# Kernel tuning notes

Hardware: AMD Instinct MI355X
Metric: run time of the kernel (lower is better)

## Reference

```python
import jax, jax.numpy as jnp
import numpy as np

EMBED_DIM = 400
NUM_HEADS = 4
HEAD_SIZE = EMBED_DIM // NUM_HEADS  # 100


def setup_inputs() -> dict:
    key = jax.random.key(0)
    ks = jax.random.split(key, 6)
    B, T = 8, 2048
    x = jax.random.normal(ks[0], (B, T, EMBED_DIM), dtype=jnp.float32)
    # per-head projection weights, stacked over heads: [H, C, D]
    scale = 1.0 / np.sqrt(EMBED_DIM)
    Wq = jax.random.normal(ks[1], (NUM_HEADS, EMBED_DIM, HEAD_SIZE), dtype=jnp.float32) * scale
    Wk = jax.random.normal(ks[2], (NUM_HEADS, EMBED_DIM, HEAD_SIZE), dtype=jnp.float32) * scale
    Wv = jax.random.normal(ks[3], (NUM_HEADS, EMBED_DIM, HEAD_SIZE), dtype=jnp.float32) * scale
    Wo = jax.random.normal(ks[4], (EMBED_DIM, EMBED_DIM), dtype=jnp.float32) * scale
    bo = jax.random.normal(ks[5], (EMBED_DIM,), dtype=jnp.float32) * scale
    return {"x": x, "Wq": Wq, "Wk": Wk, "Wv": Wv, "Wo": Wo, "bo": bo}


def reference(x, Wq, Wk, Wv, Wo, bo):
    B, T, C = x.shape
    inv_sqrt_d = 1.0 / jnp.sqrt(jnp.asarray(HEAD_SIZE, x.dtype))
    # project: [B,T,C] x [H,C,D] -> [B,H,T,D]
    q = jnp.einsum('btc,hcd->bhtd', x, Wq)
    k = jnp.einsum('btc,hcd->bhtd', x, Wk)
    v = jnp.einsum('btc,hcd->bhtd', x, Wv)
    scores = jnp.einsum('bhtd,bhsd->bhts', q, k) * inv_sqrt_d  # [B,H,T,T]
    causal = jnp.tril(jnp.ones((T, T), dtype=bool))
    scores = jnp.where(causal, scores, -jnp.inf)
    attn = jax.nn.softmax(scores, axis=-1)
    out = jnp.einsum('bhts,bhsd->bhtd', attn, v)  # [B,H,T,D]
    # concat heads (head order matches torch concat on last dim)
    out = out.transpose(0, 2, 1, 3).reshape(B, T, C)
    # output projection; dropout is identity in eval mode
    return out @ Wo.T + bo
```

## Files before the change

### kernel.cpp

```cpp
#include <hip/hip_runtime.h>
#include <hip/hip_bf16.h>

#define B_ 8
#define T_ 2048
#define C_ 400
#define H_ 4
#define D_ 100
#define DP 128
#define KP 416
#define KPB 832
#define QSCALE 0.14426950408889634f
#define MSTATIC 16.0f

typedef __hip_bfloat16 bf16;
typedef unsigned int uint32;
typedef __attribute__((ext_vector_type(8))) short short8;
typedef __attribute__((ext_vector_type(4))) float f32x4;

__device__ __forceinline__ float bf2f(bf16 v){ return __bfloat162float(v); }
__device__ __forceinline__ bf16 f2bf(float f){ return __float2bfloat16(f); }
__device__ __forceinline__ unsigned short bfbits(float f){
  bf16 h = f2bf(f);
  return __builtin_bit_cast(unsigned short, h);
}
__device__ __forceinline__ uint32 pk2(float a, float b){
  return (uint32)bfbits(a) | ((uint32)bfbits(b) << 16);
}
__device__ __forceinline__ void gl_lds16(const char* gsrc, char* ldst){
  __builtin_amdgcn_global_load_lds(
      (const __attribute__((address_space(1))) unsigned int*)gsrc,
      (__attribute__((address_space(3))) unsigned int*)ldst, 16, 0, 0);
}

__global__ __launch_bounds__(256) void conv_x_kernel(const float* __restrict__ x,
    bf16* __restrict__ xb){
  int i = blockIdx.x*256 + threadIdx.x;
  if (i >= 16384*52) return;
  int c8 = i % 52, t = i / 52;
  uint32 u[4];
  if (c8 < 50){
    const float* src = x + (size_t)t*C_ + c8*8;
    #pragma unroll
    for (int k=0;k<4;++k) u[k] = pk2(src[2*k], src[2*k+1]);
  } else {
    u[0]=u[1]=u[2]=u[3]=0;
  }
  *reinterpret_cast<uint4*>((char*)xb + (size_t)t*KPB + c8*16) = make_uint4(u[0],u[1],u[2],u[3]);
}

__global__ __launch_bounds__(256) void prep_wqkv_kernel(const float* __restrict__ Wq,
    const float* __restrict__ Wk, const float* __restrict__ Wv, bf16* __restrict__ WT){
  int i = blockIdx.x*256 + threadIdx.x;
  if (i >= 12*128*KP) return;
  int c = i % KP, n = (i/KP) & 127, group = i/(KP*128);
  int p = group >> 2, h = group & 3;
  float v = 0.f;
  if (n < D_ && c < C_){
    const float* W = (p==0)?Wq:(p==1)?Wk:Wv;
    v = W[((size_t)h*C_ + c)*D_ + n];
  }
  WT[i] = f2bf(v);
}

__global__ __launch_bounds__(256) void prep_wo_kernel(const float* __restrict__ Wo,
    bf16* __restrict__ WoB){
  int i = blockIdx.x*256 + threadIdx.x;
  if (i >= 512*KP) return;
  int c = i % KP, n = i / KP;
  float v = (n < C_ && c < C_) ? Wo[(size_t)n*C_ + c] : 0.f;
  WoB[i] = f2bf(v);
}

__global__ __launch_bounds__(256) void qkv_gemm_kernel(const bf16* __restrict__ xb,
    const bf16* __restrict__ WT, bf16* __restrict__ Qp, bf16* __restrict__ Kp,
    bf16* __restrict__ VT){
  __shared__ __align__(16) char xs[2][8192];
  __shared__ __align__(16) char wsh[2][8192];
  int bid = blockIdx.x;
  int xcd = bid & 7, idx = bid >> 3;
  int mb = xcd*16 + idx/12;
  int group = idx % 12;
  int p = group >> 2, h = group & 3;
  int t0 = mb * 128;
  int tid = threadIdx.x;
  int w = tid >> 6, l = tid & 63, g = l >> 4, qi = l & 15;
  const char* xg = (const char*)xb + (size_t)t0*KPB;
  const char* wg = (const char*)WT + (size_t)group*128*KPB;
  int srow = tid >> 2, sseg = tid & 3;

  #define GSTAGE(J, BUF) {                                                     \
    int kc2 = (J)*64;                                                          \
    _Pragma("unroll")                                                          \
    for (int r2=0;r2<2;++r2)                                                   \
      gl_lds16(xg + (size_t)(srow + r2*64)*KPB + kc2 + sseg*16,                \
               &xs[BUF][tid*16 + r2*4096]);                                    \
    _Pragma("unroll")                                                          \
    for (int r2=0;r2<2;++r2)                                                   \
      gl_lds16(wg + (size_t)(srow + r2*64)*KPB + kc2 + sseg*16,                \
               &wsh[BUF][tid*16 + r2*4096]); }

  f32x4 acc[2][8];
  #pragma unroll
  for (int mt=0;mt<2;++mt)
    #pragma unroll
    for (int nt=0;nt<8;++nt) acc[mt][nt] = (f32x4){0.f,0.f,0.f,0.f};

  GSTAGE(0, 0)
  __syncthreads();
  for (int j = 0; j < 13; ++j){
    int cur = j & 1;
    if (j < 12) GSTAGE(j+1, cur^1)
    short8 af[2];
    #pragma unroll
    for (int mt=0;mt<2;++mt)
      af[mt] = *reinterpret_cast<const short8*>(&xs[cur][(w*32 + mt*16 + qi)*64 + g*16]);
    short8 bfr[8];
    #pragma unroll
    for (int nt=0;nt<8;++nt)
      bfr[nt] = *reinterpret_cast<const short8*>(&wsh[cur][(nt*16 + qi)*64 + g*16]);
    if (p < 2){
      #pragma unroll
      for (int mt=0;mt<2;++mt)
        #pragma unroll
        for (int nt=0;nt<8;++nt)
          acc[mt][nt] = __builtin_amdgcn_mfma_f32_16x16x32_bf16(af[mt], bfr[nt], acc[mt][nt], 0,0,0);
    } else {
      #pragma unroll
      for (int mt=0;mt<2;++mt)
        #pragma unroll
        for (int nt=0;nt<8;++nt)
          acc[mt][nt] = __builtin_amdgcn_mfma_f32_16x16x32_bf16(bfr[nt], af[mt], acc[mt][nt], 0,0,0);
    }
    __syncthreads();
  }

  int b = t0 >> 11, tloc0 = t0 & 2047;
  size_t bh = (size_t)b*H_ + h;
  if (p < 2){
    float qs = (p==0) ? QSCALE : 1.0f;
    bf16* dst = (p==0 ? Qp : Kp) + (bh*T_ + tloc0)*DP;
    #pragma unroll
    for (int mt=0;mt<2;++mt)
      #pragma unroll
      for (int r=0;r<4;++r){
        int tr = w*32 + mt*16 + 4*g + r;
        #pragma unroll
        for (int nt=0;nt<8;++nt)
          dst[(size_t)tr*DP + nt*16 + qi] = f2bf(qs * acc[mt][nt][r]);
      }
  } else {
    bf16* dstv = VT + bh*DP*T_ + tloc0;
    #pragma unroll
    for (int nt=0;nt<8;++nt)
      #pragma unroll
      for (int r=0;r<4;++r){
        int d = nt*16 + 4*g + r;
        #pragma unroll
        for (int mt=0;mt<2;++mt)
          dstv[(size_t)d*T_ + w*32 + mt*16 + qi] = f2bf(acc[mt][nt][r]);
      }
  }
  #undef GSTAGE
}

__global__ __launch_bounds__(256) void out_gemm_kernel(const bf16* __restrict__ AOb,
    const bf16* __restrict__ WoB, const float* __restrict__ bo, float* __restrict__ out){
  __shared__ __align__(16) char xs[2][8192];
  __shared__ __align__(16) char wsh[2][8192];
  int bid = blockIdx.x;
  int xcd = bid & 7, idx = bid >> 3;
  int mb = xcd*16 + idx/4;
  int nb = idx & 3;
  int t0 = mb * 128, n0 = nb * 128;
  int tid = threadIdx.x;
  int w = tid >> 6, l = tid & 63, g = l >> 4, qi = l & 15;
  const char* xg = (const char*)AOb + (size_t)t0*KPB;
  const char* wg = (const char*)WoB + (size_t)n0*KPB;
  int srow = tid >> 2, sseg = tid & 3;

  #define GSTAGE(J, BUF) {                                                     \
    int kc2 = (J)*64;                                                          \
    _Pragma("unroll")                                                          \
    for (int r2=0;r2<2;++r2)                                                   \
      gl_lds16(xg + (size_t)(srow + r2*64)*KPB + kc2 + sseg*16,                \
               &xs[BUF][tid*16 + r2*4096]);                                    \
    _Pragma("unroll")                                                          \
    for (int r2=0;r2<2;++r2)                                                   \
      gl_lds16(wg + (size_t)(srow + r2*64)*KPB + kc2 + sseg*16,                \
               &wsh[BUF][tid*16 + r2*4096]); }

  f32x4 acc[2][8];
  #pragma unroll
  for (int mt=0;mt<2;++mt)
    #pragma unroll
    for (int nt=0;nt<8;++nt) acc[mt][nt] = (f32x4){0.f,0.f,0.f,0.f};

  GSTAGE(0, 0)
  __syncthreads();
  for (int j = 0; j < 13; ++j){
    int cur = j & 1;
    if (j < 12) GSTAGE(j+1, cur^1)
    short8 af[2];
    #pragma unroll
    for (int mt=0;mt<2;++mt)
      af[mt] = *reinterpret_cast<const short8*>(&xs[cur][(w*32 + mt*16 + qi)*64 + g*16]);
    short8 bfr[8];
    #pragma unroll
    for (int nt=0;nt<8;++nt)
      bfr[nt] = *reinterpret_cast<const short8*>(&wsh[cur][(nt*16 + qi)*64 + g*16]);
    #pragma unroll
    for (int mt=0;mt<2;++mt)
      #pragma unroll
      for (int nt=0;nt<8;++nt)
        acc[mt][nt] = __builtin_amdgcn_mfma_f32_16x16x32_bf16(af[mt], bfr[nt], acc[mt][nt], 0,0,0);
    __syncthreads();
  }

  #pragma unroll
  for (int nt=0;nt<8;++nt){
    if (n0 + nt*16 >= C_) continue;
    int n = n0 + nt*16 + qi;
    float bv = bo[n];
    #pragma unroll
    for (int mt=0;mt<2;++mt)
      #pragma unroll
      for (int r=0;r<4;++r){
        int tr = w*32 + mt*16 + 4*g + r;
        out[(size_t)(t0 + tr)*C_ + n] = acc[mt][nt][r] + bv;
      }
  }
  #undef GSTAGE
}

__global__ __launch_bounds__(256, 2) void attn_kernel(const bf16* __restrict__ Qp,
    const bf16* __restrict__ Kp, const bf16* __restrict__ VT, bf16* __restrict__ AOb){
  __shared__ __align__(16) char ktile[2][16384];
  __shared__ __align__(16) char vtile[2][14336];
  __shared__ __align__(16) uint32 pshare[4*2*16*36];
  const float NEGINF = -__builtin_inff();
  int bid = blockIdx.x;
  int xcd = bid & 7, idx = bid >> 3;
  int bh  = xcd*4 + (idx & 3);
  int pr  = idx >> 2;
  int qbA = pr, qbB = 31 - pr;
  int tid = threadIdx.x;
  int w = tid >> 6, l = tid & 63;
  int g = l >> 4, qi = l & 15;
  int q0A = qbA*64 + w*16, q0B = qbB*64 + w*16;
  int nchA = qbA + 1, nchB = qbB + 1;

  const bf16* Qbase = Qp + (size_t)bh*T_*DP + g*8;
  const char* Kg    = (const char*)(Kp + (size_t)bh*T_*DP);
  const char* Vg    = (const char*)(VT + (size_t)bh*DP*T_);

  short8 qfA[4], qfB[4];
  #pragma unroll
  for (int ks=0; ks<4; ++ks){
    qfA[ks] = *reinterpret_cast<const short8*>(Qbase + (size_t)(q0A + qi)*DP + ks*32);
    qfB[ks] = *reinterpret_cast<const short8*>(Qbase + (size_t)(q0B + qi)*DP + ks*32);
  }

  f32x4 accA[7], accB[7];
  #pragma unroll
  for (int dt=0; dt<7; ++dt){
    accA[dt] = (f32x4){0.f,0.f,0.f,0.f};
    accB[dt] = (f32x4){0.f,0.f,0.f,0.f};
  }
  float lrA = 0.f, lrB = 0.f;

  uint32* pbB = &pshare[((w*2 + 0)*16 + qi)*36];
  uint32* pbA = &pshare[((w*2 + 1)*16 + qi)*36];

  int st_off0 = w*4096 + l*16;
  #define STAGE(J, BUF) { int k0s = (J) << 6;                                   \
    _Pragma("unroll")                                                           \
    for (int it=0; it<4; ++it){                                                 \
      int off = st_off0 + it*1024;                                              \
      int row = off >> 8;                                                       \
      int cb  = off & 255;                                                      \
      gl_lds16(Kg + (size_t)(k0s + row)*256 + (cb ^ ((row&15)<<4)),             \
               &ktile[BUF][w*4096 + it*1024]); } }

  #define VSTAGE(J, BUF) { int k0s2 = ((J) << 6)*2;                             \
    for (int it=w; it<14; it+=4){                                               \
      int off = it*1024 + l*16;                                                 \
      int row = off >> 7;                                                       \
      int cb  = off & 127;                                                      \
      gl_lds16(Vg + (size_t)row*(T_*2) + k0s2 + (cb ^ ((row&7)<<4)),            \
               &vtile[BUF][it*1024 + l*16]); } }

  auto softpack = [&](const f32x4 st[4], float& lr, int qglob, int k0,
                      bool maskch, uint32* pb){
    float p[4][4];
    if (maskch){
      #pragma unroll
      for (int kt=0; kt<4; ++kt)
        #pragma unroll
        for (int r=0; r<4; ++r){
          int key = k0 + kt*16 + 4*g + r;
          float v = st[kt][r]; if (key > qglob) v = NEGINF;
          p[kt][r] = exp2f(v - MSTATIC);
        }
    } else {
      #pragma unroll
      for (int kt=0; kt<4; ++kt)
        #pragma unroll
        for (int r=0; r<4; ++r)
          p[kt][r] = exp2f(st[kt][r] - MSTATIC);
    }
    float rs = 0.f;
    #pragma unroll
    for (int kt=0; kt<4; ++kt)
      #pragma unroll
      for (int r=0; r<4; ++r) rs += p[kt][r];
    lr += rs;
    #pragma unroll
    for (int kt=0; kt<4; ++kt){
      pb[kt*8 + 2*g    ] = pk2(p[kt][0], p[kt][1]);
      pb[kt*8 + 2*g + 1] = pk2(p[kt][2], p[kt][3]);
    }
  };

  STAGE(0, 0)
  VSTAGE(0, 0)
  __syncthreads();

  for (int j = 0; j < nchB; ++j){
    int k0 = j << 6;
    int cur = j & 1;
    if (j + 1 < nchB){ STAGE(j+1, cur^1) VSTAGE(j+1, cur^1) }
    const char* kb = ktile[cur];
    const char* vb = vtile[cur];
    bool dual = (j < nchA);
    f32x4 stA[4], stB[4];
    __builtin_amdgcn_s_setprio(1);
    #pragma unroll
    for (int kt=0; kt<4; ++kt){
      f32x4 sB = (f32x4){0.f,0.f,0.f,0.f};
      f32x4 sA = (f32x4){0.f,0.f,0.f,0.f};
      #pragma unroll
      for (int ks=0; ks<4; ++ks){
        short8 kf = *reinterpret_cast<const short8*>(
            kb + (kt*16 + qi)*256 + ((ks*64 + g*16) ^ (qi<<4)));
        sB = __builtin_amdgcn_mfma_f32_16x16x32_bf16(kf, qfB[ks], sB, 0, 0, 0);
        if (dual)
          sA = __builtin_amdgcn_mfma_f32_16x16x32_bf16(kf, qfA[ks], sA, 0, 0, 0);
      }
      stB[kt] = sB; stA[kt] = sA;
    }
    __builtin_amdgcn_s_setprio(0);
    softpack(stB, lrB, q0B + qi, k0, j == nchB - 1, pbB);
    if (dual)
      softpack(stA, lrA, q0A + qi, k0, j == nchA - 1, pbA);
    __builtin_amdgcn_s_setprio(1);
    #pragma unroll
    for (int ks=0; ks<2; ++ks){
      short8 paB = *reinterpret_cast<const short8*>(pbB + 16*ks + 4*g);
      short8 paA = *reinterpret_cast<const short8*>(pbA + 16*ks + 4*g);
      #pragma unroll
      for (int dt=0; dt<7; ++dt){
        int row = dt*16 + qi;
        short8 vf = *reinterpret_cast<const short8*>(
            vb + row*128 + ((ks*64 + g*16) ^ ((qi&7)<<4)));
        accB[dt] = __builtin_amdgcn_mfma_f32_16x16x32_bf16(paB, vf, accB[dt], 0, 0, 0);
        if (dual)
          accA[dt] = __builtin_amdgcn_mfma_f32_16x16x32_bf16(paA, vf, accA[dt], 0, 0, 0);
      }
    }
    __builtin_amdgcn_s_setprio(0);
    __syncthreads();
  }

  lrA += __shfl_xor(lrA, 16); lrA += __shfl_xor(lrA, 32);
  lrB += __shfl_xor(lrB, 16); lrB += __shfl_xor(lrB, 32);

  int b = bh >> 2, h = bh & 3;
  #pragma unroll
  for (int tix=0; tix<2; ++tix){
    f32x4* acc = tix ? accA : accB;
    float lr = tix ? lrA : lrB;
    int q0 = tix ? q0A : q0B;
    float inv = 1.f / lr;
    float invr[4];
    #pragma unroll
    for (int r=0; r<4; ++r) invr[r] = __shfl(inv, 20*g + r);
    #pragma unroll
    for (int dt=0; dt<7; ++dt){
      int d = dt*16 + qi;
      if (d < D_){
        #pragma unroll
        for (int r=0; r<4; ++r){
          size_t row = (size_t)(b*T_) + q0 + 4*g + r;
          AOb[row*KP + h*D_ + d] = f2bf(acc[dt][r] * invr[r]);
        }
      }
    }
  }
  #undef STAGE
  #undef VSTAGE
}

extern "C" void kernel_launch(void* const* d_in, const int* in_sizes, int n_in,
                              void* d_out, int out_size, void* d_ws, size_t ws_size,
                              hipStream_t stream){
  const float* x  = (const float*)d_in[0];
  const float* Wq = (const float*)d_in[1];
  const float* Wk = (const float*)d_in[2];
  const float* Wv = (const float*)d_in[3];
  const float* Wo = (const float*)d_in[4];
  const float* bo = (const float*)d_in[5];

  constexpr size_t NBH  = (size_t)B_*H_;
  constexpr size_t NPAD = NBH*T_*DP;
  constexpr size_t NROW = (size_t)B_*T_;
  constexpr size_t OFF_QP  = 0;
  constexpr size_t OFF_KP  = OFF_QP + NPAD*2;
  constexpr size_t OFF_VT  = OFF_KP + NPAD*2;
  constexpr size_t OFF_XB  = OFF_VT + NPAD*2;
  constexpr size_t OFF_AOB = OFF_XB + NROW*KP*2;
  constexpr size_t OFF_WT  = OFF_AOB + NROW*KP*2;
  constexpr size_t OFF_WOB = OFF_WT + (size_t)12*128*KP*2;
  constexpr size_t TOTAL   = OFF_WOB + (size_t)512*KP*2;
  if (ws_size < TOTAL) return;

  char* ws = (char*)d_ws;
  bf16*  Qp   = (bf16*)(ws + OFF_QP);
  bf16*  Kp   = (bf16*)(ws + OFF_KP);
  bf16*  VTp  = (bf16*)(ws + OFF_VT);
  bf16*  xb   = (bf16*)(ws + OFF_XB);
  bf16*  AOb  = (bf16*)(ws + OFF_AOB);
  bf16*  WT   = (bf16*)(ws + OFF_WT);
  bf16*  WoB  = (bf16*)(ws + OFF_WOB);
  float* out  = (float*)d_out;

  conv_x_kernel<<<(16384*52 + 255)/256, 256, 0, stream>>>(x, xb);
  prep_wqkv_kernel<<<(12*128*KP + 255)/256, 256, 0, stream>>>(Wq, Wk, Wv, WT);
  prep_wo_kernel<<<(512*KP + 255)/256, 256, 0, stream>>>(Wo, WoB);
  qkv_gemm_kernel<<<1536, 256, 0, stream>>>(xb, WT, Qp, Kp, VTp);
  attn_kernel<<<512, 256, 0, stream>>>(Qp, Kp, VTp, AOb);
  out_gemm_kernel<<<512, 256, 0, stream>>>(AOb, WoB, bo, out);
}
```

Before: 145.4 us.

## Single-buffer K tile and share P scratch to fit three blocks per CU

```diff
diff --git a/kernel.cpp b/kernel.cpp
--- a/kernel.cpp
+++ b/kernel.cpp
@@ -232,11 +232,11 @@
   #undef GSTAGE
 }
 
-__global__ __launch_bounds__(256, 2) void attn_kernel(const bf16* __restrict__ Qp,
+__global__ __launch_bounds__(256, 3) void attn_kernel(const bf16* __restrict__ Qp,
     const bf16* __restrict__ Kp, const bf16* __restrict__ VT, bf16* __restrict__ AOb){
-  __shared__ __align__(16) char ktile[2][16384];
+  __shared__ __align__(16) char ktile[16384];
   __shared__ __align__(16) char vtile[2][14336];
-  __shared__ __align__(16) uint32 pshare[4*2*16*36];
+  __shared__ __align__(16) uint32 pshare[4*16*35];
   const float NEGINF = -__builtin_inff();
   int bid = blockIdx.x;
   int xcd = bid & 7, idx = bid >> 3;
@@ -268,18 +268,17 @@
   }
   float lrA = 0.f, lrB = 0.f;
 
-  uint32* pbB = &pshare[((w*2 + 0)*16 + qi)*36];
-  uint32* pbA = &pshare[((w*2 + 1)*16 + qi)*36];
+  uint32* pb = &pshare[(w*16 + qi)*35];
 
   int st_off0 = w*4096 + l*16;
-  #define STAGE(J, BUF) { int k0s = (J) << 6;                                   \
+  #define KSTAGE(J) { int k0s = (J) << 6;                                       \
     _Pragma("unroll")                                                           \
     for (int it=0; it<4; ++it){                                                 \
       int off = st_off0 + it*1024;                                              \
       int row = off >> 8;                                                       \
       int cb  = off & 255;                                                      \
       gl_lds16(Kg + (size_t)(k0s + row)*256 + (cb ^ ((row&15)<<4)),             \
-               &ktile[BUF][w*4096 + it*1024]); } }
+               &ktile[w*4096 + it*1024]); } }
 
   #define VSTAGE(J, BUF) { int k0s2 = ((J) << 6)*2;                             \
     for (int it=w; it<14; it+=4){                                               \
@@ -290,7 +289,7 @@
                &vtile[BUF][it*1024 + l*16]); } }
 
   auto softpack = [&](const f32x4 st[4], float& lr, int qglob, int k0,
-                      bool maskch, uint32* pb){
+                      bool maskch){
     float p[4][4];
     if (maskch){
       #pragma unroll
@@ -320,54 +319,58 @@
       pb[kt*8 + 2*g + 1] = pk2(p[kt][2], p[kt][3]);
     }
   };
-
-  STAGE(0, 0)
-  VSTAGE(0, 0)
-  __syncthreads();
-
-  for (int j = 0; j < nchB; ++j){
-    int k0 = j << 6;
-    int cur = j & 1;
-    if (j + 1 < nchB){ STAGE(j+1, cur^1) VSTAGE(j+1, cur^1) }
-    const char* kb = ktile[cur];
-    const char* vb = vtile[cur];
-    bool dual = (j < nchA);
-    f32x4 stA[4], stB[4];
-    __builtin_amdgcn_s_setprio(1);
-    #pragma unroll
-    for (int kt=0; kt<4; ++kt){
-      f32x4 sB = (f32x4){0.f,0.f,0.f,0.f};
-      f32x4 sA = (f32x4){0.f,0.f,0.f,0.f};
-      #pragma unroll
-      for (int ks=0; ks<4; ++ks){
-        short8 kf = *reinterpret_cast<const short8*>(
-            kb + (kt*16 + qi)*256 + ((ks*64 + g*16) ^ (qi<<4)));
-        sB = __builtin_amdgcn_mfma_f32_16x16x32_bf16(kf, qfB[ks], sB, 0, 0, 0);
-        if (dual)
-          sA = __builtin_amdgcn_mfma_f32_16x16x32_bf16(kf, qfA[ks], sA, 0, 0, 0);
-      }
-      stB[kt] = sB; stA[kt] = sA;
-    }
-    __builtin_amdgcn_s_setprio(0);
-    softpack(stB, lrB, q0B + qi, k0, j == nchB - 1, pbB);
-    if (dual)
-      softpack(stA, lrA, q0A + qi, k0, j == nchA - 1, pbA);
-    __builtin_amdgcn_s_setprio(1);
+  auto pv = [&](const char* vb, f32x4 acc[7]){
     #pragma unroll
     for (int ks=0; ks<2; ++ks){
-      short8 paB = *reinterpret_cast<const short8*>(pbB + 16*ks + 4*g);
-      short8 paA = *reinterpret_cast<const short8*>(pbA + 16*ks + 4*g);
+      short8 pa = *reinterpret_cast<const short8*>(pb + 16*ks + 4*g);
       #pragma unroll
       for (int dt=0; dt<7; ++dt){
         int row = dt*16 + qi;
         short8 vf = *reinterpret_cast<const short8*>(
             vb + row*128 + ((ks*64 + g*16) ^ ((qi&7)<<4)));
-        accB[dt] = __builtin_amdgcn_mfma_f32_16x16x32_bf16(paB, vf, accB[dt], 0, 0, 0);
+        acc[dt] = __builtin_amdgcn_mfma_f32_16x16x32_bf16(pa, vf, acc[dt], 0, 0, 0);
+      }
+    }
+  };
+
+  KSTAGE(0)
+  VSTAGE(0, 0)
+  __syncthreads();
+
+  for (int j = 0; j < nchB; ++j){
+    int k0 = j << 6;
+    int cur = j & 1;
+    bool dual = (j < nchA);
+    f32x4 stA[4], stB[4];
+    __builtin_amdgcn_s_setprio(1);
+    #pragma unroll
+    for (int kt=0; kt<4; ++kt){
+      f32x4 sB = (f32x4){0.f,0.f,0.f,0.f};
+      f32x4 sA = (f32x4){0.f,0.f,0.f,0.f};
+      #pragma unroll
+      for (int ks=0; ks<4; ++ks){
+        short8 kf = *reinterpret_cast<const short8*>(
+            ktile + (kt*16 + qi)*256 + ((ks*64 + g*16) ^ (qi<<4)));
+        sB = __builtin_amdgcn_mfma_f32_16x16x32_bf16(kf, qfB[ks], sB, 0, 0, 0);
         if (dual)
-          accA[dt] = __builtin_amdgcn_mfma_f32_16x16x32_bf16(paA, vf, accA[dt], 0, 0, 0);
-      }
+          sA = __builtin_amdgcn_mfma_f32_16x16x32_bf16(kf, qfA[ks], sA, 0, 0, 0);
+      }
+      stB[kt] = sB; stA[kt] = sA;
     }
     __builtin_amdgcn_s_setprio(0);
+    __syncthreads();
+    if (j + 1 < nchB){ KSTAGE(j+1) VSTAGE(j+1, cur^1) }
+    const char* vb = vtile[cur];
+    softpack(stB, lrB, q0B + qi, k0, j == nchB - 1);
+    __builtin_amdgcn_s_setprio(1);
+    pv(vb, accB);
+    __builtin_amdgcn_s_setprio(0);
+    if (dual){
+      softpack(stA, lrA, q0A + qi, k0, j == nchA - 1);
+      __builtin_amdgcn_s_setprio(1);
+      pv(vb, accA);
+      __builtin_amdgcn_s_setprio(0);
+    }
     __syncthreads();
   }
 
@@ -396,7 +399,7 @@
       }
     }
   }
-  #undef STAGE
+  #undef KSTAGE
   #undef VSTAGE
 }
 
```

Result: slower. 164.1 us (+12.9%).

## Load V fragments directly from global into registers, raise attention occupancy

Applied to the files above, without the earlier changes.

```diff
diff --git a/kernel.cpp b/kernel.cpp
--- a/kernel.cpp
+++ b/kernel.cpp
@@ -48,27 +48,27 @@
   *reinterpret_cast<uint4*>((char*)xb + (size_t)t*KPB + c8*16) = make_uint4(u[0],u[1],u[2],u[3]);
 }
 
-__global__ __launch_bounds__(256) void prep_wqkv_kernel(const float* __restrict__ Wq,
-    const float* __restrict__ Wk, const float* __restrict__ Wv, bf16* __restrict__ WT){
+__global__ __launch_bounds__(256) void prep_w_kernel(const float* __restrict__ Wq,
+    const float* __restrict__ Wk, const float* __restrict__ Wv,
+    const float* __restrict__ Wo, bf16* __restrict__ WT, bf16* __restrict__ WoB){
   int i = blockIdx.x*256 + threadIdx.x;
-  if (i >= 12*128*KP) return;
-  int c = i % KP, n = (i/KP) & 127, group = i/(KP*128);
-  int p = group >> 2, h = group & 3;
-  float v = 0.f;
-  if (n < D_ && c < C_){
-    const float* W = (p==0)?Wq:(p==1)?Wk:Wv;
-    v = W[((size_t)h*C_ + c)*D_ + n];
-  }
-  WT[i] = f2bf(v);
-}
-
-__global__ __launch_bounds__(256) void prep_wo_kernel(const float* __restrict__ Wo,
-    bf16* __restrict__ WoB){
-  int i = blockIdx.x*256 + threadIdx.x;
-  if (i >= 512*KP) return;
-  int c = i % KP, n = i / KP;
-  float v = (n < C_ && c < C_) ? Wo[(size_t)n*C_ + c] : 0.f;
-  WoB[i] = f2bf(v);
+  if (i < 12*128*KP){
+    int c = i % KP, n = (i/KP) & 127, group = i/(KP*128);
+    int p = group >> 2, h = group & 3;
+    float v = 0.f;
+    if (n < D_ && c < C_){
+      const float* W = (p==0)?Wq:(p==1)?Wk:Wv;
+      v = W[((size_t)h*C_ + c)*D_ + n];
+    }
+    WT[i] = f2bf(v);
+  } else {
+    int k = i - 12*128*KP;
+    if (k < 512*KP){
+      int c = k % KP, n = k / KP;
+      float v = (n < C_ && c < C_) ? Wo[(size_t)n*C_ + c] : 0.f;
+      WoB[k] = f2bf(v);
+    }
+  }
 }
 
 __global__ __launch_bounds__(256) void qkv_gemm_kernel(const bf16* __restrict__ xb,
@@ -232,10 +232,9 @@
   #undef GSTAGE
 }
 
-__global__ __launch_bounds__(256, 2) void attn_kernel(const bf16* __restrict__ Qp,
+__global__ __launch_bounds__(256, 3) void attn_kernel(const bf16* __restrict__ Qp,
     const bf16* __restrict__ Kp, const bf16* __restrict__ VT, bf16* __restrict__ AOb){
   __shared__ __align__(16) char ktile[2][16384];
-  __shared__ __align__(16) char vtile[2][14336];
   __shared__ __align__(16) uint32 pshare[4*2*16*36];
   const float NEGINF = -__builtin_inff();
   int bid = blockIdx.x;
@@ -272,7 +271,7 @@
   uint32* pbA = &pshare[((w*2 + 1)*16 + qi)*36];
 
   int st_off0 = w*4096 + l*16;
-  #define STAGE(J, BUF) { int k0s = (J) << 6;                                   \
+  #define KSTAGE(J, BUF) { int k0s = (J) << 6;                                  \
     _Pragma("unroll")                                                           \
     for (int it=0; it<4; ++it){                                                 \
       int off = st_off0 + it*1024;                                              \
@@ -281,14 +280,6 @@
       gl_lds16(Kg + (size_t)(k0s + row)*256 + (cb ^ ((row&15)<<4)),             \
                &ktile[BUF][w*4096 + it*1024]); } }
 
-  #define VSTAGE(J, BUF) { int k0s2 = ((J) << 6)*2;                             \
-    for (int it=w; it<14; it+=4){                                               \
-      int off = it*1024 + l*16;                                                 \
-      int row = off >> 7;                                                       \
-      int cb  = off & 127;                                                      \
-      gl_lds16(Vg + (size_t)row*(T_*2) + k0s2 + (cb ^ ((row&7)<<4)),            \
-               &vtile[BUF][it*1024 + l*16]); } }
-
   auto softpack = [&](const f32x4 st[4], float& lr, int qglob, int k0,
                       bool maskch, uint32* pb){
     float p[4][4];
@@ -321,16 +312,21 @@
     }
   };
 
-  STAGE(0, 0)
-  VSTAGE(0, 0)
+  KSTAGE(0, 0)
   __syncthreads();
 
   for (int j = 0; j < nchB; ++j){
     int k0 = j << 6;
     int cur = j & 1;
-    if (j + 1 < nchB){ STAGE(j+1, cur^1) VSTAGE(j+1, cur^1) }
+    if (j + 1 < nchB) KSTAGE(j+1, cur^1)
+    short8 vr[14];
+    #pragma unroll
+    for (int ks=0; ks<2; ++ks)
+      #pragma unroll
+      for (int dt=0; dt<7; ++dt)
+        vr[ks*7 + dt] = *reinterpret_cast<const short8*>(
+            Vg + (size_t)(dt*16 + qi)*(T_*2) + (size_t)(k0 + ks*32 + g*8)*2);
     const char* kb = ktile[cur];
-    const char* vb = vtile[cur];
     bool dual = (j < nchA);
     f32x4 stA[4], stB[4];
     __builtin_amdgcn_s_setprio(1);
@@ -359,9 +355,7 @@
       short8 paA = *reinterpret_cast<const short8*>(pbA + 16*ks + 4*g);
       #pragma unroll
       for (int dt=0; dt<7; ++dt){
-        int row = dt*16 + qi;
-        short8 vf = *reinterpret_cast<const short8*>(
-            vb + row*128 + ((ks*64 + g*16) ^ ((qi&7)<<4)));
+        short8 vf = vr[ks*7 + dt];
         accB[dt] = __builtin_amdgcn_mfma_f32_16x16x32_bf16(paB, vf, accB[dt], 0, 0, 0);
         if (dual)
           accA[dt] = __builtin_amdgcn_mfma_f32_16x16x32_bf16(paA, vf, accA[dt], 0, 0, 0);
@@ -396,8 +390,7 @@
       }
     }
   }
-  #undef STAGE
-  #undef VSTAGE
+  #undef KSTAGE
 }
 
 extern "C" void kernel_launch(void* const* d_in, const int* in_sizes, int n_in,
@@ -434,8 +427,7 @@
   float* out  = (float*)d_out;
 
   conv_x_kernel<<<(16384*52 + 255)/256, 256, 0, stream>>>(x, xb);
-  prep_wqkv_kernel<<<(12*128*KP + 255)/256, 256, 0, stream>>>(Wq, Wk, Wv, WT);
-  prep_wo_kernel<<<(512*KP + 255)/256, 256, 0, stream>>>(Wo, WoB);
+  prep_w_kernel<<<3328, 256, 0, stream>>>(Wq, Wk, Wv, Wo, WT, WoB);
   qkv_gemm_kernel<<<1536, 256, 0, stream>>>(xb, WT, Qp, Kp, VTp);
   attn_kernel<<<512, 256, 0, stream>>>(Qp, Kp, VTp, AOb);
   out_gemm_kernel<<<512, 256, 0, stream>>>(AOb, WoB, bo, out);
```

After: 343.6 us. 2.36x slower.
